# Optimization experiments

Hardware: AMD Instinct MI355X
Metric: run time of the kernel (lower is better)

The kernel has to match this reference:

```python
import jax, jax.numpy as jnp
import numpy as np

N_NODES = 100000
N_EDGES = 1600000
IN_CH = 128
OUT_CH = 128
HEADS = 4
HEAD_DIM = OUT_CH // HEADS
NEG_SLOPE_ATT = 0.2   # GATConv default negative_slope
NEG_SLOPE_ACT = 0.2   # block's LeakyReLU(0.2)
BN_EPS = 1e-5


def setup_inputs() -> dict:
    key = jax.random.key(0)
    ks = jax.random.split(key, 6)
    x = jax.random.normal(ks[0], (N_NODES, IN_CH), dtype=jnp.float32)
    edge_index = jax.random.randint(ks[1], (2, N_EDGES), 0, N_NODES, dtype=jnp.int64)
    W = jax.random.normal(ks[2], (IN_CH, HEADS * HEAD_DIM), dtype=jnp.float32) * (1.0 / np.sqrt(IN_CH))
    att_src = jax.random.normal(ks[3], (HEADS, HEAD_DIM), dtype=jnp.float32) * 0.1
    att_dst = jax.random.normal(ks[4], (HEADS, HEAD_DIM), dtype=jnp.float32) * 0.1
    bias = jnp.zeros((OUT_CH,), dtype=jnp.float32)
    gamma = jnp.ones((OUT_CH,), dtype=jnp.float32)
    beta = jnp.zeros((OUT_CH,), dtype=jnp.float32)
    return {"x": x, "edge_index": edge_index, "W": W, "att_src": att_src,
            "att_dst": att_dst, "bias": bias, "gamma": gamma, "beta": beta}


def reference(x, edge_index, W, att_src, att_dst, bias, gamma, beta):
    N = x.shape[0]
    H, C = att_src.shape
    src, dst = edge_index[0], edge_index[1]

    # linear projection per head: [N, H, C]
    h = (x @ W).reshape(N, H, C)

    # per-node attention contributions (alpha_src[i] + alpha_dst[j] on edges)
    a_src = jnp.einsum('nhc,hc->nh', h, att_src)  # [N, H]
    a_dst = jnp.einsum('nhc,hc->nh', h, att_dst)  # [N, H]

    # per-edge raw score, leaky relu (GAT attention nonlinearity)
    e = jax.nn.leaky_relu(a_src[src] + a_dst[dst], NEG_SLOPE_ATT)  # [E, H]

    # segment softmax over edges grouped by destination node
    e_max = jax.ops.segment_max(e, dst, num_segments=N)            # [N, H]
    e_max = jnp.where(jnp.isfinite(e_max), e_max, 0.0)
    ex = jnp.exp(e - e_max[dst])                                   # [E, H]
    denom = jax.ops.segment_sum(ex, dst, num_segments=N)           # [N, H]
    alpha = ex / (denom[dst] + 1e-16)                              # [E, H]

    # scatter-add aggregation of alpha-weighted source features
    msg = alpha[:, :, None] * h[src]                               # [E, H, C]
    out = jax.ops.segment_sum(msg, dst, num_segments=N)            # [N, H, C]
    out = out.reshape(N, H * C) + bias                             # concat heads + bias

    # BatchNorm1d (training mode: batch statistics, biased variance)
    mu = out.mean(axis=0)
    var = out.var(axis=0)
    out = (out - mu) * jax.lax.rsqrt(var + BN_EPS) * gamma + beta

    return jax.nn.leaky_relu(out, NEG_SLOPE_ACT)
```

## Files before the change

### kernel.cpp

```cpp
#include <hip/hip_runtime.h>
#include <hip/hip_fp16.h>
#include <math.h>


#define WAVE  64
#define SHIFT 8
#define CAP   4608
#define CPAD  16

__device__ __forceinline__ float4 leaky4(float4 v, float s) {
    v.x = v.x > 0.f ? v.x : s * v.x;
    v.y = v.y > 0.f ? v.y : s * v.y;
    v.z = v.z > 0.f ? v.z : s * v.z;
    v.w = v.w > 0.f ? v.w : s * v.w;
    return v;
}

__global__ __launch_bounds__(256) void k_gemm_att(
    const float* __restrict__ x, const float* __restrict__ W,
    const float* __restrict__ att_src, const float* __restrict__ att_dst,
    __half* __restrict__ h16, float* __restrict__ a_src, float* __restrict__ a_dst,
    int N)
{
    __shared__ float xsT[128][36];
    __shared__ float Wl[64][128];

    const int t = threadIdx.x;
    const int row0 = blockIdx.x * 32;

    {
        const int r  = t >> 3;
        const int k0 = (t & 7) * 16;
        const int rr = min(row0 + r, N - 1);
        const float4* xp = (const float4*)(x + (size_t)rr * 128 + k0);
        float4 v0 = xp[0], v1 = xp[1], v2 = xp[2], v3 = xp[3];
        float tmp[16] = {v0.x,v0.y,v0.z,v0.w, v1.x,v1.y,v1.z,v1.w,
                         v2.x,v2.y,v2.z,v2.w, v3.x,v3.y,v3.z,v3.w};
        #pragma unroll
        for (int i = 0; i < 16; ++i) xsT[k0 + i][r] = tmp[i];
    }

    const int tx = t & 31;
    const int ty = t >> 5;
    float acc[4][4] = {{0.f}};

    for (int kt = 0; kt < 2; ++kt) {
        __syncthreads();
        {
            const float4* wp = (const float4*)(W + kt * 64 * 128);
            float4* wl = (float4*)&Wl[0][0];
            #pragma unroll
            for (int i = 0; i < 8; ++i) wl[t + 256 * i] = wp[t + 256 * i];
        }
        __syncthreads();
        #pragma unroll
        for (int k = 0; k < 64; ++k) {
            float4 wv = *(const float4*)&Wl[k][tx * 4];
            float4 xv = *(const float4*)&xsT[kt * 64 + k][ty * 4];
            float xa[4] = {xv.x, xv.y, xv.z, xv.w};
            float wa[4] = {wv.x, wv.y, wv.z, wv.w};
            #pragma unroll
            for (int i = 0; i < 4; ++i)
                #pragma unroll
                for (int j = 0; j < 4; ++j)
                    acc[i][j] = fmaf(xa[i], wa[j], acc[i][j]);
        }
    }

    const int head = tx >> 3;
    const float4 s4 = *(const float4*)&att_src[head * 32 + (tx & 7) * 4];
    const float4 d4 = *(const float4*)&att_dst[head * 32 + (tx & 7) * 4];

    #pragma unroll
    for (int i = 0; i < 4; ++i) {
        const int n = row0 + ty * 4 + i;
        if (n < N) {
            union { __half2 h2[2]; uint2 u; } pk;
            pk.h2[0] = __floats2half2_rn(acc[i][0], acc[i][1]);
            pk.h2[1] = __floats2half2_rn(acc[i][2], acc[i][3]);
            *(uint2*)(h16 + (size_t)n * 128 + tx * 4) = pk.u;
        }
        float ss = acc[i][0]*s4.x + acc[i][1]*s4.y + acc[i][2]*s4.z + acc[i][3]*s4.w;
        float dd = acc[i][0]*d4.x + acc[i][1]*d4.y + acc[i][2]*d4.z + acc[i][3]*d4.w;
        #pragma unroll
        for (int off = 1; off < 8; off <<= 1) {
            ss += __shfl_xor(ss, off);
            dd += __shfl_xor(dd, off);
        }
        if ((tx & 7) == 0 && n < N) {
            a_src[n * 4 + head] = ss;
            a_dst[n * 4 + head] = dd;
        }
    }
}

__global__ __launch_bounds__(256) void k_bucket(
    const int* __restrict__ src, const int* __restrict__ dst,
    int* __restrict__ cursor, int2* __restrict__ pairs, int E, int nbkt)
{
    __shared__ int hist[512];
    __shared__ int lcur[512];
    const int t = threadIdx.x;
    hist[t] = 0; hist[t + 256] = 0;
    __syncthreads();

    const int base = blockIdx.x * 2048;
    int sr[8], dr[8];
    #pragma unroll
    for (int i = 0; i < 8; ++i) {
        const int e = base + i * 256 + t;
        if (e < E) { sr[i] = src[e]; dr[i] = dst[e]; }
        else       { sr[i] = -1;     dr[i] = -1; }
    }
    #pragma unroll
    for (int i = 0; i < 8; ++i)
        if (dr[i] >= 0) atomicAdd(&hist[dr[i] >> SHIFT], 1);
    __syncthreads();

    for (int b = t; b < nbkt; b += 256) {
        const int hcount = hist[b];
        lcur[b] = (hcount > 0) ? atomicAdd(&cursor[b * CPAD], hcount) + b * CAP
                               : b * CAP;
    }
    __syncthreads();

    #pragma unroll
    for (int i = 0; i < 8; ++i) {
        if (dr[i] >= 0) {
            const int b = dr[i] >> SHIFT;
            const int pos = atomicAdd(&lcur[b], 1);
            if (pos < b * CAP + CAP)
                pairs[pos] = make_int2(sr[i], dr[i]);
        }
    }
}

__global__ __launch_bounds__(256) void k_fine(
    const int* __restrict__ cursor, const int2* __restrict__ pairs,
    int* __restrict__ offsets, int* __restrict__ deg,
    int* __restrict__ perm_src, int N)
{
    __shared__ int cnt[256];
    __shared__ int scn[256];
    __shared__ int cur[256];

    const int t = threadIdx.x;
    const int b = blockIdx.x;
    const int cnt_b = min(cursor[b * CPAD], CAP);
    const int pbase = b * CAP;

    cnt[t] = 0;
    __syncthreads();

    for (int i = t; i < cnt_b; i += 256) {
        const int2 p = pairs[pbase + i];
        atomicAdd(&cnt[p.y & 255], 1);
    }
    __syncthreads();

    const int v = cnt[t];
    scn[t] = v;
    __syncthreads();
    for (int off = 1; off < 256; off <<= 1) {
        const int add = (t >= off) ? scn[t - off] : 0;
        __syncthreads();
        scn[t] += add;
        __syncthreads();
    }
    const int excl = scn[t] - v;

    const int node = (b << SHIFT) + t;
    if (node < N) {
        offsets[node] = pbase + excl;
        deg[node]     = v;
    }
    cur[t] = pbase + excl;
    __syncthreads();

    for (int i = t; i < cnt_b; i += 256) {
        const int2 p = pairs[pbase + i];
        const int pos = atomicAdd(&cur[p.y & 255], 1);
        perm_src[pos] = p.x;
    }
}

__global__ __launch_bounds__(256) void k_aggregate(
    const int* __restrict__ offsets, const int* __restrict__ deg,
    const int* __restrict__ perm_src,
    const float* __restrict__ a_src, const float* __restrict__ a_dst,
    const __half* __restrict__ h16, float* __restrict__ out, int N)
{
    __shared__ int   ls_s [4][64];
    __shared__ float ls_ex[4][4][64];

    const int wv   = threadIdx.x >> 6;
    const int lane = threadIdx.x & 63;
    const int n = blockIdx.x * 4 + wv;
    if (n >= N) return;

    const int beg = offsets[n];
    const int dg  = deg[n];
    const float4 ad = *(const float4*)(a_dst + n * 4);

    const int ch = lane * 2;
    const int hd = lane >> 4;
    float2 acc = make_float2(0.f, 0.f);
    float dsum = 0.f;

    for (int base = 0; base < dg; base += WAVE) {
        const int idx = base + lane;
        int s = 0;
        float4 ex = make_float4(0.f, 0.f, 0.f, 0.f);
        if (idx < dg) {
            s = perm_src[beg + idx];
            float4 as = *(const float4*)(a_src + s * 4);
            float4 e = leaky4(make_float4(as.x+ad.x, as.y+ad.y, as.z+ad.z, as.w+ad.w), 0.2f);
            ex.x = __expf(e.x); ex.y = __expf(e.y);
            ex.z = __expf(e.z); ex.w = __expf(e.w);
        }
        ls_s [wv][lane]    = s;
        ls_ex[wv][0][lane] = ex.x;
        ls_ex[wv][1][lane] = ex.y;
        ls_ex[wv][2][lane] = ex.z;
        ls_ex[wv][3][lane] = ex.w;
        const int cn = min(WAVE, dg - base);
        for (int j = 0; j < cn; ++j) {
            int   sj  = ls_s [wv][j];
            float exj = ls_ex[wv][hd][j];
            float2 hv = __half22float2(*(const __half2*)(h16 + (size_t)sj * 128 + ch));
            acc.x = fmaf(exj, hv.x, acc.x);
            acc.y = fmaf(exj, hv.y, acc.y);
            dsum += exj;
        }
    }

    const float inv = 1.0f / (dsum + 1e-16f);
    *(float2*)(out + (size_t)n * 128 + ch) = make_float2(acc.x * inv, acc.y * inv);
}

__global__ __launch_bounds__(256) void k_bnstats(const float* __restrict__ out,
                                                 float* __restrict__ sums, int N)
{
    const int c    = threadIdx.x & 127;
    const int half = threadIdx.x >> 7;
    float s = 0.f, sq = 0.f;
    for (int r = blockIdx.x * 2 + half; r < N; r += gridDim.x * 2) {
        float v = out[(size_t)r * 128 + c];
        s += v;
        sq = fmaf(v, v, sq);
    }
    __shared__ float ls[256], lq[256];
    ls[threadIdx.x] = s; lq[threadIdx.x] = sq;
    __syncthreads();
    if (half == 0) {
        s  += ls[threadIdx.x + 128];
        sq += lq[threadIdx.x + 128];
        atomicAdd(&sums[c], s);
        atomicAdd(&sums[128 + c], sq);
    }
}

__global__ __launch_bounds__(256) void k_bnapply(float* __restrict__ out,
                                                 const float* __restrict__ sums,
                                                 const float* __restrict__ gamma,
                                                 const float* __restrict__ beta,
                                                 int N)
{
    const int i = blockIdx.x * 256 + threadIdx.x;
    const int total = N * 128;
    if (i >= total) return;
    const int c = i & 127;
    const float invN = 1.0f / (float)N;
    float mu  = sums[c] * invN;
    float var = sums[128 + c] * invN - mu * mu;
    float v = out[i];
    float y = (v - mu) * rsqrtf(var + 1e-5f) * gamma[c] + beta[c];
    out[i] = y > 0.f ? y : 0.2f * y;
}

extern "C" void kernel_launch(void* const* d_in, const int* in_sizes, int n_in,
                              void* d_out, int out_size, void* d_ws, size_t ws_size,
                              hipStream_t stream)
{
    const float* x     = (const float*)d_in[0];
    const int*   ei    = (const int*)  d_in[1];
    const float* W     = (const float*)d_in[2];
    const float* att_s = (const float*)d_in[3];
    const float* att_d = (const float*)d_in[4];
    const float* gamma = (const float*)d_in[6];
    const float* beta  = (const float*)d_in[7];
    float* out = (float*)d_out;

    const int N = in_sizes[0] / 128;
    const int E = in_sizes[1] / 2;
    const int nbkt = (N + (1 << SHIFT) - 1) >> SHIFT;

    char* ws = (char*)d_ws;
    size_t off = 0;
    auto carve = [&](size_t bytes) {
        char* p = ws + off;
        off += (bytes + 255) & ~(size_t)255;
        return p;
    };
    __half* h16      = (__half*)carve((size_t)N * 128 * 2);
    float* a_src     = (float*)carve((size_t)N * 4 * 4);
    float* a_dst     = (float*)carve((size_t)N * 4 * 4);
    int*   offsets   = (int*)  carve((size_t)N * 4);
    int*   deg       = (int*)  carve((size_t)N * 4);
    int*   cursor    = (int*)  carve((size_t)nbkt * CPAD * 4);
    float* bn_sums   = (float*)carve(256 * 4);
    int2*  pairs     = (int2*) carve((size_t)nbkt * CAP * 8);
    int*   perm_src  = (int*)  carve((size_t)nbkt * CAP * 4);

    hipMemsetAsync(cursor, 0, (size_t)nbkt * CPAD * 4, stream);
    hipMemsetAsync(bn_sums, 0, 256 * 4, stream);

    k_gemm_att<<<(N + 31) / 32, 256, 0, stream>>>(x, W, att_s, att_d, h16, a_src, a_dst, N);
    k_bucket<<<(E + 2047) / 2048, 256, 0, stream>>>(ei, ei + E, cursor, pairs, E, nbkt);
    k_fine<<<nbkt, 256, 0, stream>>>(cursor, pairs, offsets, deg, perm_src, N);
    k_aggregate<<<(N + 3) / 4, 256, 0, stream>>>(offsets, deg, perm_src, a_src, a_dst, h16, out, N);
    k_bnstats<<<512, 256, 0, stream>>>(out, bn_sums, N);
    k_bnapply<<<(N * 128 + 255) / 256, 256, 0, stream>>>(out, bn_sums, gamma, beta, N);
}
```

Before: 349.2 us.

## Pack two nodes per wave in aggregation with 16-byte loads and split edges

The aggregation kernel now has each 64-lane wave handle two destination nodes, one per 32-lane half. Within a half, 16 lanes read a full 128-channel fp16 row using 16-byte vector loads. The two 16-lane groups take alternating edges and combine their partial sums with a shuffle at the end. This replaces one node per wave with narrow 4-byte loads, and aims for fewer loop iterations and more memory-level parallelism on the gather of source features. The cost is padded iterations, since loop trip counts are rounded up and set to the maximum degree of the paired nodes, plus extra shuffles and registers.

```diff
diff --git a/kernel.cpp b/kernel.cpp
--- a/kernel.cpp
+++ b/kernel.cpp
@@ -190,25 +190,32 @@
     const float* __restrict__ a_src, const float* __restrict__ a_dst,
     const __half* __restrict__ h16, float* __restrict__ out, int N)
 {
-    __shared__ int   ls_s [4][64];
-    __shared__ float ls_ex[4][4][64];
+    __shared__ int    ls_s [4][2][32];
+    __shared__ float4 ls_ex[4][2][32];
 
     const int wv   = threadIdx.x >> 6;
     const int lane = threadIdx.x & 63;
-    const int n = blockIdx.x * 4 + wv;
-    if (n >= N) return;
-
-    const int beg = offsets[n];
-    const int dg  = deg[n];
-    const float4 ad = *(const float4*)(a_dst + n * 4);
-
-    const int ch = lane * 2;
-    const int hd = lane >> 4;
-    float2 acc = make_float2(0.f, 0.f);
+    const int nd   = lane >> 5;
+    const int l32  = lane & 31;
+    const int n    = blockIdx.x * 8 + wv * 2 + nd;
+    const bool valid = (n < N);
+
+    const int beg = valid ? offsets[n] : 0;
+    const int dg  = valid ? deg[n]     : 0;
+    const float4 ad = valid ? *(const float4*)(a_dst + n * 4)
+                            : make_float4(0.f, 0.f, 0.f, 0.f);
+
+    const int ph  = (lane >> 4) & 1;
+    const int l16 = lane & 15;
+    const int ch  = l16 * 8;
+    const int hd  = l16 >> 2;
+    float acc[8] = {0.f,0.f,0.f,0.f,0.f,0.f,0.f,0.f};
     float dsum = 0.f;
 
-    for (int base = 0; base < dg; base += WAVE) {
-        const int idx = base + lane;
+    const int dgmax = max(dg, __shfl_xor(dg, 32));
+
+    for (int base = 0; base < dgmax; base += 32) {
+        const int idx = base + l32;
         int s = 0;
         float4 ex = make_float4(0.f, 0.f, 0.f, 0.f);
         if (idx < dg) {
@@ -218,24 +225,43 @@
             ex.x = __expf(e.x); ex.y = __expf(e.y);
             ex.z = __expf(e.z); ex.w = __expf(e.w);
         }
-        ls_s [wv][lane]    = s;
-        ls_ex[wv][0][lane] = ex.x;
-        ls_ex[wv][1][lane] = ex.y;
-        ls_ex[wv][2][lane] = ex.z;
-        ls_ex[wv][3][lane] = ex.w;
-        const int cn = min(WAVE, dg - base);
-        for (int j = 0; j < cn; ++j) {
-            int   sj  = ls_s [wv][j];
-            float exj = ls_ex[wv][hd][j];
-            float2 hv = __half22float2(*(const __half2*)(h16 + (size_t)sj * 128 + ch));
-            acc.x = fmaf(exj, hv.x, acc.x);
-            acc.y = fmaf(exj, hv.y, acc.y);
+        ls_s [wv][nd][l32] = s;
+        ls_ex[wv][nd][l32] = ex;
+
+        int cn = dg - base;
+        cn = (cn < 0) ? 0 : ((cn > 32) ? 32 : cn);
+        const int cnmax = max(cn, __shfl_xor(cn, 32));
+        const int cnr = (cnmax + 3) & ~3;
+
+        #pragma unroll 2
+        for (int t = 0; t < cnr; t += 2) {
+            const int slot = t + ph;
+            const int   sj  = ls_s[wv][nd][slot];
+            const float exj = ((const float*)&ls_ex[wv][nd][slot])[hd];
+            union { uint4 u; __half2 h2[4]; } pk;
+            pk.u = *(const uint4*)(h16 + (size_t)sj * 128 + ch);
+            acc[0] = fmaf(__low2float (pk.h2[0]), exj, acc[0]);
+            acc[1] = fmaf(__high2float(pk.h2[0]), exj, acc[1]);
+            acc[2] = fmaf(__low2float (pk.h2[1]), exj, acc[2]);
+            acc[3] = fmaf(__high2float(pk.h2[1]), exj, acc[3]);
+            acc[4] = fmaf(__low2float (pk.h2[2]), exj, acc[4]);
+            acc[5] = fmaf(__high2float(pk.h2[2]), exj, acc[5]);
+            acc[6] = fmaf(__low2float (pk.h2[3]), exj, acc[6]);
+            acc[7] = fmaf(__high2float(pk.h2[3]), exj, acc[7]);
             dsum += exj;
         }
     }
 
-    const float inv = 1.0f / (dsum + 1e-16f);
-    *(float2*)(out + (size_t)n * 128 + ch) = make_float2(acc.x * inv, acc.y * inv);
+    #pragma unroll
+    for (int c = 0; c < 8; ++c) acc[c] += __shfl_xor(acc[c], 16);
+    dsum += __shfl_xor(dsum, 16);
+
+    if (ph == 0 && valid) {
+        const float inv = 1.0f / (dsum + 1e-16f);
+        float* op = out + (size_t)n * 128 + ch;
+        *(float4*)(op)     = make_float4(acc[0]*inv, acc[1]*inv, acc[2]*inv, acc[3]*inv);
+        *(float4*)(op + 4) = make_float4(acc[4]*inv, acc[5]*inv, acc[6]*inv, acc[7]*inv);
+    }
 }
 
 __global__ __launch_bounds__(256) void k_bnstats(const float* __restrict__ out,
@@ -318,7 +344,7 @@
     k_gemm_att<<<(N + 31) / 32, 256, 0, stream>>>(x, W, att_s, att_d, h16, a_src, a_dst, N);
     k_bucket<<<(E + 2047) / 2048, 256, 0, stream>>>(ei, ei + E, cursor, pairs, E, nbkt);
     k_fine<<<nbkt, 256, 0, stream>>>(cursor, pairs, offsets, deg, perm_src, N);
-    k_aggregate<<<(N + 3) / 4, 256, 0, stream>>>(offsets, deg, perm_src, a_src, a_dst, h16, out, N);
+    k_aggregate<<<(N + 7) / 8, 256, 0, stream>>>(offsets, deg, perm_src, a_src, a_dst, h16, out, N);
     k_bnstats<<<512, 256, 0, stream>>>(out, bn_sums, N);
     k_bnapply<<<(N * 128 + 255) / 256, 256, 0, stream>>>(out, bn_sums, gamma, beta, N);
 }
```

Measured after the change: 345.6 us. Within noise of the previous version (-1.0%).
